# Optimization experiments

Measured on AMD Instinct MI355X. Metric: run time of the kernel, lower is better.

The kernel has to match this reference:

```python
import jax, jax.numpy as jnp
import numpy as np

B, K, N, F_IN, F_OUT, T = 32, 3, 512, 64, 64, 64


def setup_inputs() -> dict:
    key = jax.random.key(0)
    ks = jax.random.split(key, 6)
    x = jax.random.normal(ks[0], (B, N, F_IN, T), dtype=jnp.float32)
    spatial_attention_scores = jax.random.normal(ks[1], (B, K, N, N), dtype=jnp.float32)
    adj_pa_static = jax.random.uniform(ks[2], (N, N), dtype=jnp.float32)
    # Chebyshev polynomial buffers T_k(L~), one [N,N] per order
    cheb_T = jax.random.normal(ks[3], (K, N, N), dtype=jnp.float32) / np.sqrt(N)
    # Xavier-uniform-ish init for Theta and per-k masks
    lim_t = float(np.sqrt(6.0 / (F_IN + F_OUT)))
    Theta = jax.random.uniform(ks[4], (K, F_IN, F_OUT), dtype=jnp.float32, minval=-lim_t, maxval=lim_t)
    lim_m = float(np.sqrt(6.0 / (N + N)))
    mask = jax.random.uniform(ks[5], (K, N, N), dtype=jnp.float32, minval=-lim_m, maxval=lim_m)
    return {"x": x, "spatial_attention_scores": spatial_attention_scores,
            "adj_pa_static": adj_pa_static, "cheb_T": cheb_T, "Theta": Theta, "mask": mask}


def reference(x, spatial_attention_scores, adj_pa_static, cheb_T, Theta, mask):
    # x: [B,N,F_in,T]; scores: [B,K,N,N]; adj: [N,N]; cheb_T: [K,N,N];
    # Theta: [K,F_in,F_out]; mask: [K,N,N]
    # Spatial factors are timestep-independent -> compute once.
    dyn = adj_pa_static[None, :, :] * mask                     # [K,N,N]
    combined = spatial_attention_scores + dyn[None]            # [B,K,N,N]
    A = jax.nn.softmax(combined, axis=-1)                      # softmax over neighbors (torch dim=2 of [B,N,N])
    A_eff = cheb_T[None] * A                                   # [B,K,N,N]
    # sum_k (A_eff_k @ x_t) @ Theta_k, fused over all timesteps and orders
    out = jnp.einsum('bknm,bmit,kio->bnot', A_eff, x, Theta)   # [B,N,F_out,T]
    return jax.nn.relu(out)
```

## Files before the change

kernel.cpp:

```cpp
#include <hip/hip_runtime.h>
#include <hip/hip_bf16.h>

#define BATCH 32
#define KC 3
#define NP 512
#define FIN 64
#define FOUT 64
#define TP 64
#define COLS (FOUT*TP)
#define KDIM (KC*NP)

typedef unsigned short ushort_t;
typedef __attribute__((ext_vector_type(8))) short short8;
typedef __attribute__((ext_vector_type(4))) float f32x4;

__device__ __forceinline__ unsigned short f2bf(float f) {
    unsigned u = __float_as_uint(f);
    return (unsigned short)((u + 0x7FFF + ((u >> 16) & 1)) >> 16);
}
__device__ __forceinline__ float bf2f(unsigned short h) {
    return __uint_as_float(((unsigned)h) << 16);
}

#define GLDS16(g, l)                                                          \
    __builtin_amdgcn_global_load_lds(                                         \
        (const __attribute__((address_space(1))) void*)(g),                   \
        (__attribute__((address_space(3))) void*)(l), 16, 0, 0)

__global__ __launch_bounds__(256) void k_softmax(
    const float* __restrict__ scores, const float* __restrict__ adj,
    const float* __restrict__ mask, const float* __restrict__ cheb,
    unsigned short* __restrict__ Ah, unsigned short* __restrict__ Al, int b0)
{
    const int n = blockIdx.x;
    const int k = blockIdx.y;
    const int c = blockIdx.z;
    const int b = b0 + c;
    const int tid = threadIdx.x;
    const size_t srow = (((size_t)b*KC + k)*NP + n)*NP;
    const size_t krow = ((size_t)k*NP + n)*NP;
    const size_t arow = (size_t)n*NP;

    float v0 = scores[srow+tid]     + adj[arow+tid]    *mask[krow+tid];
    float v1 = scores[srow+tid+256] + adj[arow+tid+256]*mask[krow+tid+256];

    float mx = fmaxf(v0, v1);
    #pragma unroll
    for (int off=32; off>0; off>>=1) mx = fmaxf(mx, __shfl_down(mx, off, 64));
    __shared__ float rmax[4], rsum[4];
    const int wv = tid>>6, ln = tid&63;
    if (ln==0) rmax[wv] = mx;
    __syncthreads();
    mx = fmaxf(fmaxf(rmax[0],rmax[1]), fmaxf(rmax[2],rmax[3]));

    const float e0 = __expf(v0-mx), e1 = __expf(v1-mx);
    float s = e0+e1;
    #pragma unroll
    for (int off=32; off>0; off>>=1) s += __shfl_down(s, off, 64);
    if (ln==0) rsum[wv] = s;
    __syncthreads();
    const float inv = 1.0f/(rsum[0]+rsum[1]+rsum[2]+rsum[3]);

    const size_t orow = (((size_t)c*KC + k)*NP + n)*NP;
    float a0 = cheb[krow+tid]    *e0*inv;
    float a1 = cheb[krow+tid+256]*e1*inv;
    unsigned short h0 = f2bf(a0), h1 = f2bf(a1);
    unsigned short l0 = f2bf(a0 - bf2f(h0)), l1 = f2bf(a1 - bf2f(h1));
    Ah[orow+tid]     = h0;  Al[orow+tid]     = l0;
    Ah[orow+tid+256] = h1;  Al[orow+tid+256] = l1;
}

__global__ __launch_bounds__(256) void k_xt(
    const float* __restrict__ x,
    unsigned short* __restrict__ Xth, unsigned short* __restrict__ Xtl, int b0)
{
    __shared__ float Ls[64][68];
    const int m0 = blockIdx.x*64, col0 = blockIdx.y*64, c = blockIdx.z;
    const int b = b0 + c;
    const float* xb = x + (size_t)b*NP*COLS;
    const int tid = threadIdx.x;
    const int r = tid >> 4, f4 = tid & 15;
    #pragma unroll
    for (int j=0;j<4;j++) {
        float4 v = *(const float4*)&xb[(size_t)(m0 + r + j*16)*COLS + col0 + f4*4];
        *(float4*)&Ls[r + j*16][f4*4] = v;
    }
    __syncthreads();
    const int oc = tid >> 2, seg = tid & 3;
    unsigned short h[16], l[16];
    #pragma unroll
    for (int u=0;u<16;u++) {
        float f = Ls[seg*16 + u][oc];
        h[u] = f2bf(f);
        l[u] = f2bf(f - bf2f(h[u]));
    }
    size_t off = ((size_t)c*COLS + col0 + oc)*NP + m0 + seg*16;
    *(uint4*)&Xth[off]   = *(const uint4*)&h[0];
    *(uint4*)&Xth[off+8] = *(const uint4*)&h[8];
    *(uint4*)&Xtl[off]   = *(const uint4*)&l[0];
    *(uint4*)&Xtl[off+8] = *(const uint4*)&l[8];
}

__global__ __launch_bounds__(256) void k_gemm(
    const unsigned short* __restrict__ Ah, const unsigned short* __restrict__ Al,
    const unsigned short* __restrict__ Xth, const unsigned short* __restrict__ Xtl,
    float* __restrict__ Y)
{
    __shared__ __align__(16) unsigned short Ash[2][128*32];
    __shared__ __align__(16) unsigned short Asl[2][128*32];
    __shared__ __align__(16) unsigned short Bsh[2][128*32];
    __shared__ __align__(16) unsigned short Bsl[2][128*32];

    const int tid  = threadIdx.x;
    const int lane = tid & 63, wave = tid >> 6;
    const int wr = wave >> 1, wc = wave & 1;
    const int lr = lane & 15, quad = lane >> 4;

    const int Cg   = gridDim.y;
    const int flat = blockIdx.x + 384 * blockIdx.y;
    const int c    = flat % Cg;
    const int rr   = flat / Cg;
    const int colg = rr / 48;
    const int rem  = rr % 48;
    const int kn   = rem >> 2;
    const int colb = colg*4 + (rem & 3);
    const int k    = kn % 3;
    const int nb   = kn / 3;
    const int n0   = nb * 128, col0 = colb * 128;

    const unsigned short* Ah_ = Ah  + ((size_t)(c*KC + k)*NP)*NP;
    const unsigned short* Al_ = Al  + ((size_t)(c*KC + k)*NP)*NP;
    const unsigned short* Bh_ = Xth + (size_t)c*COLS*NP;
    const unsigned short* Bl_ = Xtl + (size_t)c*COLS*NP;

    f32x4 acc[4][4];
    #pragma unroll
    for (int i=0;i<4;i++)
        #pragma unroll
        for (int j=0;j<4;j++)
            acc[i][j] = (f32x4){0.f,0.f,0.f,0.f};

    const int sr  = tid >> 2;
    const int qsw = (((tid & 3) ^ ((tid >> 3) & 3)) * 8);
    const int rq  = (quad ^ ((lr >> 1) & 3)) * 8;

    auto STAGE = [&](int bb, int m0) {
        const unsigned short* gah = Ah_ + ((size_t)(n0 + sr))*NP + m0 + qsw;
        const unsigned short* gal = Al_ + ((size_t)(n0 + sr))*NP + m0 + qsw;
        const unsigned short* gbh = Bh_ + ((size_t)(col0 + sr))*NP + m0 + qsw;
        const unsigned short* gbl = Bl_ + ((size_t)(col0 + sr))*NP + m0 + qsw;
        GLDS16(gah,          &Ash[bb][tid*8]);
        GLDS16(gah + 64*NP,  &Ash[bb][2048 + tid*8]);
        GLDS16(gal,          &Asl[bb][tid*8]);
        GLDS16(gal + 64*NP,  &Asl[bb][2048 + tid*8]);
        GLDS16(gbh,          &Bsh[bb][tid*8]);
        GLDS16(gbh + 64*NP,  &Bsh[bb][2048 + tid*8]);
        GLDS16(gbl,          &Bsl[bb][tid*8]);
        GLDS16(gbl + 64*NP,  &Bsl[bb][2048 + tid*8]);
    };

    STAGE(0, 0);
    int bb = 0;

    #pragma unroll 1
    for (int t = 0; t < NP/32; ++t) {
        __syncthreads();
        if (t+1 < NP/32) STAGE(bb^1, 32*(t+1));

        short8 ah[4], al[4], bh[4], bl[4];
        #pragma unroll
        for (int i=0;i<4;i++) {
            const int ra = (wr*64 + i*16 + lr)*32 + rq;
            ah[i] = *(const short8*)&Ash[bb][ra];
            al[i] = *(const short8*)&Asl[bb][ra];
        }
        #pragma unroll
        for (int j=0;j<4;j++) {
            const int rb = (wc*64 + j*16 + lr)*32 + rq;
            bh[j] = *(const short8*)&Bsh[bb][rb];
            bl[j] = *(const short8*)&Bsl[bb][rb];
        }
        #pragma unroll
        for (int i=0;i<4;i++)
            #pragma unroll
            for (int j=0;j<4;j++) {
                acc[i][j] = __builtin_amdgcn_mfma_f32_16x16x32_bf16(
                    ah[i], bh[j], acc[i][j], 0, 0, 0);
                acc[i][j] = __builtin_amdgcn_mfma_f32_16x16x32_bf16(
                    al[i], bh[j], acc[i][j], 0, 0, 0);
                acc[i][j] = __builtin_amdgcn_mfma_f32_16x16x32_bf16(
                    ah[i], bl[j], acc[i][j], 0, 0, 0);
            }
        bb ^= 1;
    }

    float* Yc = Y + ((size_t)(c*KC + k)*NP + n0 + wr*64)*COLS + col0 + wc*64;
    #pragma unroll
    for (int i=0;i<4;i++) {
        #pragma unroll
        for (int r=0;r<4;r++) {
            const size_t row_off = (size_t)(i*16 + quad*4 + r)*COLS;
            #pragma unroll
            for (int j=0;j<4;j++)
                Yc[row_off + j*16 + lr] = acc[i][j][r];
        }
    }
}

__global__ __launch_bounds__(256) void k_theta(
    const float* __restrict__ Y, const float* __restrict__ Theta,
    float* __restrict__ out, int b0)
{
    __shared__ __align__(16) float Ys[KC*FIN*TP];
    const int n = blockIdx.x, c = blockIdx.y;
    const int tid = threadIdx.x;

    #pragma unroll
    for (int j=0;j<12;j++) {
        int f4  = tid + j*256;
        int lin = f4*4;
        int kk  = lin >> 12;
        int off = lin & 4095;
        ((float4*)Ys)[f4] =
            *(const float4*)&Y[((size_t)(c*KC + kk)*NP + n)*COLS + off];
    }
    __syncthreads();

    const int o = tid & 63, tw = tid >> 6;
    float4 a0 = {0,0,0,0}, a1 = a0, a2 = a0, a3 = a0;

    #pragma unroll 8
    for (int ki = 0; ki < KC*FIN; ++ki) {
        float th = Theta[ki*FOUT + o];
        const float* ys = &Ys[ki*TP + tw*16];
        float4 y0 = *(const float4*)&ys[0];
        float4 y1 = *(const float4*)&ys[4];
        float4 y2 = *(const float4*)&ys[8];
        float4 y3 = *(const float4*)&ys[12];
        a0.x += th*y0.x; a0.y += th*y0.y; a0.z += th*y0.z; a0.w += th*y0.w;
        a1.x += th*y1.x; a1.y += th*y1.y; a1.z += th*y1.z; a1.w += th*y1.w;
        a2.x += th*y2.x; a2.y += th*y2.y; a2.z += th*y2.z; a2.w += th*y2.w;
        a3.x += th*y3.x; a3.y += th*y3.y; a3.z += th*y3.z; a3.w += th*y3.w;
    }

    float* og = out + (((size_t)(b0 + c)*NP + n)*FOUT + o)*TP + tw*16;
    float4 r0 = make_float4(fmaxf(a0.x,0.f), fmaxf(a0.y,0.f), fmaxf(a0.z,0.f), fmaxf(a0.w,0.f));
    float4 r1 = make_float4(fmaxf(a1.x,0.f), fmaxf(a1.y,0.f), fmaxf(a1.z,0.f), fmaxf(a1.w,0.f));
    float4 r2 = make_float4(fmaxf(a2.x,0.f), fmaxf(a2.y,0.f), fmaxf(a2.z,0.f), fmaxf(a2.w,0.f));
    float4 r3 = make_float4(fmaxf(a3.x,0.f), fmaxf(a3.y,0.f), fmaxf(a3.z,0.f), fmaxf(a3.w,0.f));
    *(float4*)&og[0]  = r0;
    *(float4*)&og[4]  = r1;
    *(float4*)&og[8]  = r2;
    *(float4*)&og[12] = r3;
}

extern "C" void kernel_launch(void* const* d_in, const int* in_sizes, int n_in,
                              void* d_out, int out_size, void* d_ws, size_t ws_size,
                              hipStream_t stream)
{
    const float* x      = (const float*)d_in[0];
    const float* scores = (const float*)d_in[1];
    const float* adj    = (const float*)d_in[2];
    const float* cheb   = (const float*)d_in[3];
    const float* Theta  = (const float*)d_in[4];
    const float* mask   = (const float*)d_in[5];
    float* out = (float*)d_out;

    const size_t eA = (size_t)KC*NP*NP;
    const size_t eX = (size_t)COLS*NP;
    const size_t eY = (size_t)KC*NP*COLS;
    const size_t perB = 2*eA*2 + 2*eX*2 + eY*4;

    int C = (int)(ws_size / perB);
    if (C < 1) C = 1;
    if (C > 8) C = 8;
    while (BATCH % C) C--;

    char* p = (char*)d_ws;
    unsigned short* Ah  = (unsigned short*)p;  p += (size_t)C*eA*2;
    unsigned short* Al  = (unsigned short*)p;  p += (size_t)C*eA*2;
    unsigned short* Xth = (unsigned short*)p;  p += (size_t)C*eX*2;
    unsigned short* Xtl = (unsigned short*)p;  p += (size_t)C*eX*2;
    float*          Yw  = (float*)p;

    for (int b0 = 0; b0 < BATCH; b0 += C) {
        k_softmax<<<dim3(NP, KC, C),  256, 0, stream>>>(scores, adj, mask, cheb, Ah, Al, b0);
        k_xt     <<<dim3(NP/64, COLS/64, C), 256, 0, stream>>>(x, Xth, Xtl, b0);
        k_gemm   <<<dim3(384, C),     256, 0, stream>>>(Ah, Al, Xth, Xtl, Yw);
        k_theta  <<<dim3(NP, C),      256, 0, stream>>>(Yw, Theta, out, b0);
    }
}
```

Baseline: 1.642 ms.

## Drop x low-part split, store Y as fp16, fuse prep kernels, widen batch chunk

Removes the bf16 low-part split of x, so the GEMM does two MFMAs per tile instead of three and skips staging the Xtl tile. The intermediate Y is stored as fp16 with nontemporal stores and widened back to fp32 in the theta kernel, halving that buffer's traffic. The softmax and transpose kernels are merged into one launch, and the batch chunk limit is raised to the full batch, with a new block-to-batch mapping. This trades accuracy, since x is rounded to bf16 and Y to fp16, for less compute, memory traffic and launch overhead.

```diff
diff --git a/kernel.cpp b/kernel.cpp
--- a/kernel.cpp
+++ b/kernel.cpp
@@ -27,89 +27,81 @@
         (const __attribute__((address_space(1))) void*)(g),                   \
         (__attribute__((address_space(3))) void*)(l), 16, 0, 0)
 
-__global__ __launch_bounds__(256) void k_softmax(
+__global__ __launch_bounds__(256) void k_prep(
     const float* __restrict__ scores, const float* __restrict__ adj,
     const float* __restrict__ mask, const float* __restrict__ cheb,
-    unsigned short* __restrict__ Ah, unsigned short* __restrict__ Al, int b0)
-{
-    const int n = blockIdx.x;
-    const int k = blockIdx.y;
-    const int c = blockIdx.z;
+    const float* __restrict__ x,
+    unsigned short* __restrict__ Ah, unsigned short* __restrict__ Al,
+    unsigned short* __restrict__ Xth, int b0)
+{
+    __shared__ float Ls[64][68];
+    __shared__ float rmax[4], rsum[4];
+    const int c = blockIdx.y;
     const int b = b0 + c;
     const int tid = threadIdx.x;
-    const size_t srow = (((size_t)b*KC + k)*NP + n)*NP;
-    const size_t krow = ((size_t)k*NP + n)*NP;
-    const size_t arow = (size_t)n*NP;
-
-    float v0 = scores[srow+tid]     + adj[arow+tid]    *mask[krow+tid];
-    float v1 = scores[srow+tid+256] + adj[arow+tid+256]*mask[krow+tid+256];
-
-    float mx = fmaxf(v0, v1);
-    #pragma unroll
-    for (int off=32; off>0; off>>=1) mx = fmaxf(mx, __shfl_down(mx, off, 64));
-    __shared__ float rmax[4], rsum[4];
-    const int wv = tid>>6, ln = tid&63;
-    if (ln==0) rmax[wv] = mx;
-    __syncthreads();
-    mx = fmaxf(fmaxf(rmax[0],rmax[1]), fmaxf(rmax[2],rmax[3]));
-
-    const float e0 = __expf(v0-mx), e1 = __expf(v1-mx);
-    float s = e0+e1;
-    #pragma unroll
-    for (int off=32; off>0; off>>=1) s += __shfl_down(s, off, 64);
-    if (ln==0) rsum[wv] = s;
-    __syncthreads();
-    const float inv = 1.0f/(rsum[0]+rsum[1]+rsum[2]+rsum[3]);
-
-    const size_t orow = (((size_t)c*KC + k)*NP + n)*NP;
-    float a0 = cheb[krow+tid]    *e0*inv;
-    float a1 = cheb[krow+tid+256]*e1*inv;
-    unsigned short h0 = f2bf(a0), h1 = f2bf(a1);
-    unsigned short l0 = f2bf(a0 - bf2f(h0)), l1 = f2bf(a1 - bf2f(h1));
-    Ah[orow+tid]     = h0;  Al[orow+tid]     = l0;
-    Ah[orow+tid+256] = h1;  Al[orow+tid+256] = l1;
-}
-
-__global__ __launch_bounds__(256) void k_xt(
-    const float* __restrict__ x,
-    unsigned short* __restrict__ Xth, unsigned short* __restrict__ Xtl, int b0)
-{
-    __shared__ float Ls[64][68];
-    const int m0 = blockIdx.x*64, col0 = blockIdx.y*64, c = blockIdx.z;
-    const int b = b0 + c;
-    const float* xb = x + (size_t)b*NP*COLS;
-    const int tid = threadIdx.x;
-    const int r = tid >> 4, f4 = tid & 15;
-    #pragma unroll
-    for (int j=0;j<4;j++) {
-        float4 v = *(const float4*)&xb[(size_t)(m0 + r + j*16)*COLS + col0 + f4*4];
-        *(float4*)&Ls[r + j*16][f4*4] = v;
-    }
-    __syncthreads();
-    const int oc = tid >> 2, seg = tid & 3;
-    unsigned short h[16], l[16];
-    #pragma unroll
-    for (int u=0;u<16;u++) {
-        float f = Ls[seg*16 + u][oc];
-        h[u] = f2bf(f);
-        l[u] = f2bf(f - bf2f(h[u]));
-    }
-    size_t off = ((size_t)c*COLS + col0 + oc)*NP + m0 + seg*16;
-    *(uint4*)&Xth[off]   = *(const uint4*)&h[0];
-    *(uint4*)&Xth[off+8] = *(const uint4*)&h[8];
-    *(uint4*)&Xtl[off]   = *(const uint4*)&l[0];
-    *(uint4*)&Xtl[off+8] = *(const uint4*)&l[8];
+
+    if (blockIdx.x < KC*NP) {
+        const int n = blockIdx.x & (NP-1);
+        const int k = blockIdx.x >> 9;
+        const size_t srow = (((size_t)b*KC + k)*NP + n)*NP;
+        const size_t krow = ((size_t)k*NP + n)*NP;
+        const size_t arow = (size_t)n*NP;
+
+        float v0 = scores[srow+tid]     + adj[arow+tid]    *mask[krow+tid];
+        float v1 = scores[srow+tid+256] + adj[arow+tid+256]*mask[krow+tid+256];
+
+        float mx = fmaxf(v0, v1);
+        #pragma unroll
+        for (int off=32; off>0; off>>=1) mx = fmaxf(mx, __shfl_down(mx, off, 64));
+        const int wv = tid>>6, ln = tid&63;
+        if (ln==0) rmax[wv] = mx;
+        __syncthreads();
+        mx = fmaxf(fmaxf(rmax[0],rmax[1]), fmaxf(rmax[2],rmax[3]));
+
+        const float e0 = __expf(v0-mx), e1 = __expf(v1-mx);
+        float s = e0+e1;
+        #pragma unroll
+        for (int off=32; off>0; off>>=1) s += __shfl_down(s, off, 64);
+        if (ln==0) rsum[wv] = s;
+        __syncthreads();
+        const float inv = 1.0f/(rsum[0]+rsum[1]+rsum[2]+rsum[3]);
+
+        const size_t orow = (((size_t)c*KC + k)*NP + n)*NP;
+        float a0 = cheb[krow+tid]    *e0*inv;
+        float a1 = cheb[krow+tid+256]*e1*inv;
+        unsigned short h0 = f2bf(a0), h1 = f2bf(a1);
+        unsigned short l0 = f2bf(a0 - bf2f(h0)), l1 = f2bf(a1 - bf2f(h1));
+        Ah[orow+tid]     = h0;  Al[orow+tid]     = l0;
+        Ah[orow+tid+256] = h1;  Al[orow+tid+256] = l1;
+    } else {
+        const int t = blockIdx.x - KC*NP;
+        const int m0 = (t & 7)*64, col0 = (t >> 3)*64;
+        const float* xb = x + (size_t)b*NP*COLS;
+        const int r = tid >> 4, f4 = tid & 15;
+        #pragma unroll
+        for (int j=0;j<4;j++) {
+            float4 v = *(const float4*)&xb[(size_t)(m0 + r + j*16)*COLS + col0 + f4*4];
+            *(float4*)&Ls[r + j*16][f4*4] = v;
+        }
+        __syncthreads();
+        const int oc = tid >> 2, seg = tid & 3;
+        unsigned short h[16];
+        #pragma unroll
+        for (int u=0;u<16;u++) h[u] = f2bf(Ls[seg*16 + u][oc]);
+        size_t off = ((size_t)c*COLS + col0 + oc)*NP + m0 + seg*16;
+        *(uint4*)&Xth[off]   = *(const uint4*)&h[0];
+        *(uint4*)&Xth[off+8] = *(const uint4*)&h[8];
+    }
 }
 
 __global__ __launch_bounds__(256) void k_gemm(
     const unsigned short* __restrict__ Ah, const unsigned short* __restrict__ Al,
-    const unsigned short* __restrict__ Xth, const unsigned short* __restrict__ Xtl,
-    float* __restrict__ Y)
+    const unsigned short* __restrict__ Xth,
+    _Float16* __restrict__ Y)
 {
     __shared__ __align__(16) unsigned short Ash[2][128*32];
     __shared__ __align__(16) unsigned short Asl[2][128*32];
     __shared__ __align__(16) unsigned short Bsh[2][128*32];
-    __shared__ __align__(16) unsigned short Bsl[2][128*32];
 
     const int tid  = threadIdx.x;
     const int lane = tid & 63, wave = tid >> 6;
@@ -118,8 +110,15 @@
 
     const int Cg   = gridDim.y;
     const int flat = blockIdx.x + 384 * blockIdx.y;
-    const int c    = flat % Cg;
-    const int rr   = flat / Cg;
+    int c, rr;
+    if (Cg >= 8) {
+        const int s = flat & 7, t = flat >> 3;
+        rr = t % 384;
+        c  = s + 8 * (t / 384);
+    } else {
+        c  = flat % Cg;
+        rr = flat / Cg;
+    }
     const int colg = rr / 48;
     const int rem  = rr % 48;
     const int kn   = rem >> 2;
@@ -131,7 +130,6 @@
     const unsigned short* Ah_ = Ah  + ((size_t)(c*KC + k)*NP)*NP;
     const unsigned short* Al_ = Al  + ((size_t)(c*KC + k)*NP)*NP;
     const unsigned short* Bh_ = Xth + (size_t)c*COLS*NP;
-    const unsigned short* Bl_ = Xtl + (size_t)c*COLS*NP;
 
     f32x4 acc[4][4];
     #pragma unroll
@@ -148,15 +146,12 @@
         const unsigned short* gah = Ah_ + ((size_t)(n0 + sr))*NP + m0 + qsw;
         const unsigned short* gal = Al_ + ((size_t)(n0 + sr))*NP + m0 + qsw;
         const unsigned short* gbh = Bh_ + ((size_t)(col0 + sr))*NP + m0 + qsw;
-        const unsigned short* gbl = Bl_ + ((size_t)(col0 + sr))*NP + m0 + qsw;
         GLDS16(gah,          &Ash[bb][tid*8]);
         GLDS16(gah + 64*NP,  &Ash[bb][2048 + tid*8]);
         GLDS16(gal,          &Asl[bb][tid*8]);
         GLDS16(gal + 64*NP,  &Asl[bb][2048 + tid*8]);
         GLDS16(gbh,          &Bsh[bb][tid*8]);
         GLDS16(gbh + 64*NP,  &Bsh[bb][2048 + tid*8]);
-        GLDS16(gbl,          &Bsl[bb][tid*8]);
-        GLDS16(gbl + 64*NP,  &Bsl[bb][2048 + tid*8]);
     };
 
     STAGE(0, 0);
@@ -167,7 +162,7 @@
         __syncthreads();
         if (t+1 < NP/32) STAGE(bb^1, 32*(t+1));
 
-        short8 ah[4], al[4], bh[4], bl[4];
+        short8 ah[4], al[4], bh[4];
         #pragma unroll
         for (int i=0;i<4;i++) {
             const int ra = (wr*64 + i*16 + lr)*32 + rq;
@@ -178,7 +173,6 @@
         for (int j=0;j<4;j++) {
             const int rb = (wc*64 + j*16 + lr)*32 + rq;
             bh[j] = *(const short8*)&Bsh[bb][rb];
-            bl[j] = *(const short8*)&Bsl[bb][rb];
         }
         #pragma unroll
         for (int i=0;i<4;i++)
@@ -188,27 +182,29 @@
                     ah[i], bh[j], acc[i][j], 0, 0, 0);
                 acc[i][j] = __builtin_amdgcn_mfma_f32_16x16x32_bf16(
                     al[i], bh[j], acc[i][j], 0, 0, 0);
-                acc[i][j] = __builtin_amdgcn_mfma_f32_16x16x32_bf16(
-                    ah[i], bl[j], acc[i][j], 0, 0, 0);
             }
         bb ^= 1;
     }
 
-    float* Yc = Y + ((size_t)(c*KC + k)*NP + n0 + wr*64)*COLS + col0 + wc*64;
+    _Float16* Yc = Y + ((size_t)(c*KC + k)*NP + n0 + wr*64)*COLS + col0 + wc*64;
     #pragma unroll
     for (int i=0;i<4;i++) {
         #pragma unroll
         for (int r=0;r<4;r++) {
             const size_t row_off = (size_t)(i*16 + quad*4 + r)*COLS;
             #pragma unroll
-            for (int j=0;j<4;j++)
-                Yc[row_off + j*16 + lr] = acc[i][j][r];
+            for (int j=0;j<4;j++) {
+                _Float16 hv = (_Float16)acc[i][j][r];
+                __builtin_nontemporal_store(
+                    __builtin_bit_cast(unsigned short, hv),
+                    (unsigned short*)&Yc[row_off + j*16 + lr]);
+            }
         }
     }
 }
 
 __global__ __launch_bounds__(256) void k_theta(
-    const float* __restrict__ Y, const float* __restrict__ Theta,
+    const _Float16* __restrict__ Y, const float* __restrict__ Theta,
     float* __restrict__ out, int b0)
 {
     __shared__ __align__(16) float Ys[KC*FIN*TP];
@@ -216,13 +212,16 @@
     const int tid = threadIdx.x;
 
     #pragma unroll
-    for (int j=0;j<12;j++) {
-        int f4  = tid + j*256;
-        int lin = f4*4;
-        int kk  = lin >> 12;
-        int off = lin & 4095;
-        ((float4*)Ys)[f4] =
-            *(const float4*)&Y[((size_t)(c*KC + kk)*NP + n)*COLS + off];
+    for (int j=0;j<6;j++) {
+        int idx8 = (tid + j*256)*8;
+        int kk   = idx8 >> 12;
+        int off  = idx8 & 4095;
+        union { uint4 u; _Float16 h[8]; } v;
+        v.u = *(const uint4*)&Y[((size_t)(c*KC + kk)*NP + n)*COLS + off];
+        float4 lo = make_float4((float)v.h[0], (float)v.h[1], (float)v.h[2], (float)v.h[3]);
+        float4 hi = make_float4((float)v.h[4], (float)v.h[5], (float)v.h[6], (float)v.h[7]);
+        *(float4*)&Ys[idx8]     = lo;
+        *(float4*)&Ys[idx8 + 4] = hi;
     }
     __syncthreads();
 
@@ -269,24 +268,22 @@
     const size_t eA = (size_t)KC*NP*NP;
     const size_t eX = (size_t)COLS*NP;
     const size_t eY = (size_t)KC*NP*COLS;
-    const size_t perB = 2*eA*2 + 2*eX*2 + eY*4;
+    const size_t perB = 2*eA*2 + eX*2 + eY*2;
 
     int C = (int)(ws_size / perB);
     if (C < 1) C = 1;
-    if (C > 8) C = 8;
+    if (C > BATCH) C = BATCH;
     while (BATCH % C) C--;
 
     char* p = (char*)d_ws;
     unsigned short* Ah  = (unsigned short*)p;  p += (size_t)C*eA*2;
     unsigned short* Al  = (unsigned short*)p;  p += (size_t)C*eA*2;
     unsigned short* Xth = (unsigned short*)p;  p += (size_t)C*eX*2;
-    unsigned short* Xtl = (unsigned short*)p;  p += (size_t)C*eX*2;
-    float*          Yw  = (float*)p;
+    _Float16*       Yw  = (_Float16*)p;
 
     for (int b0 = 0; b0 < BATCH; b0 += C) {
-        k_softmax<<<dim3(NP, KC, C),  256, 0, stream>>>(scores, adj, mask, cheb, Ah, Al, b0);
-        k_xt     <<<dim3(NP/64, COLS/64, C), 256, 0, stream>>>(x, Xth, Xtl, b0);
-        k_gemm   <<<dim3(384, C),     256, 0, stream>>>(Ah, Al, Xth, Xtl, Yw);
-        k_theta  <<<dim3(NP, C),      256, 0, stream>>>(Yw, Theta, out, b0);
-    }
-}
+        k_prep <<<dim3(KC*NP + 512, C), 256, 0, stream>>>(scores, adj, mask, cheb, x, Ah, Al, Xth, b0);
+        k_gemm <<<dim3(384, C),         256, 0, stream>>>(Ah, Al, Xth, Yw);
+        k_theta<<<dim3(NP, C),          256, 0, stream>>>(Yw, Theta, out, b0);
+    }
+}
```

Result: faster. 1.315 ms (-19.9%).
